# Performance work log

Measured on AMD Instinct MI355X. Metric: run time of the kernel, lower is better.

Reference implementation:

```python
import jax, jax.numpy as jnp
import numpy as np
import math


def _rope(x, cos, sin):
    # x: [B, S, h, hd]; cos/sin: [S, hd//2]
    B, S, h, hd = x.shape
    xr = x.reshape(B, S, h, hd // 2, 2)
    x_re, x_im = xr[..., 0], xr[..., 1]
    c = cos[None, :, None, :]
    s = sin[None, :, None, :]
    out_re = x_re * c - x_im * s
    out_im = x_re * s + x_im * c
    return jnp.stack([out_re, out_im], axis=-1).reshape(B, S, h, hd)


def setup_inputs() -> dict:
    key = jax.random.key(0)
    ks = jax.random.split(key, 8)
    B, S, D = 2, 2048, 2048
    H, G = 16, 4
    hd = D // H  # 128
    q = jax.random.normal(ks[0], (B, S, D), dtype=jnp.float32)
    k = jax.random.normal(ks[1], (B, S, D), dtype=jnp.float32)
    v = jax.random.normal(ks[2], (B, S, D), dtype=jnp.float32)
    # causal mask, matching typical usage (mask==0 -> -inf)
    mask = jnp.broadcast_to(jnp.tril(jnp.ones((S, S), dtype=jnp.int32)), (B, S, S))
    # RoPE freqs: thetas = base**(-2*arange(0,hd,2)/hd), freq = outer(m, thetas)
    exp = -2.0 * jnp.arange(0, hd, 2, dtype=jnp.float32) / hd
    thetas = jnp.power(10000.0, exp)
    m = jnp.arange(S, dtype=jnp.float32)
    freq = jnp.outer(m, thetas)  # [S, hd//2]
    freq_cos = jnp.cos(freq)
    freq_sin = jnp.sin(freq)
    sc = 0.02
    W_q = jax.random.normal(ks[3], (D, D), dtype=jnp.float32) * sc
    W_k = jax.random.normal(ks[4], (D, D // G), dtype=jnp.float32) * sc
    W_v = jax.random.normal(ks[5], (D, D // G), dtype=jnp.float32) * sc
    W_o = jax.random.normal(ks[6], (D, D), dtype=jnp.float32) * sc
    return {"q": q, "k": k, "v": v, "mask": mask, "freq_cos": freq_cos,
            "freq_sin": freq_sin, "W_q": W_q, "W_k": W_k, "W_v": W_v,
            "W_o": W_o, "heads": 16, "group_size": 4}


def reference(q, k, v, mask, freq_cos, freq_sin, W_q, W_k, W_v, W_o, heads, group_size):
    B, S, D = q.shape
    H = heads
    Hkv = H // group_size
    hd = D // H
    qp = (q @ W_q).reshape(B, S, H, hd)
    kp = (k @ W_k).reshape(B, S, Hkv, hd)
    vp = (v @ W_v).reshape(B, S, Hkv, hd)
    qp = _rope(qp, freq_cos, freq_sin)
    kp = _rope(kp, freq_cos, freq_sin)
    # repeat_kv: each kv head repeated group_size times (group index inner)
    kp = jnp.repeat(kp, group_size, axis=2)  # [B,S,H,hd]
    vp = jnp.repeat(vp, group_size, axis=2)
    qh = qp.transpose(0, 2, 1, 3)  # [B,H,S,hd]
    kh = kp.transpose(0, 2, 1, 3)
    vh = vp.transpose(0, 2, 1, 3)
    scores = jnp.einsum('bhqd,bhkd->bhqk', qh, kh) / math.sqrt(hd)
    scores = jnp.where(mask[:, None, :, :] == 0, jnp.float32(-1e9), scores)
    attn = jax.nn.softmax(scores, axis=-1)
    out = jnp.einsum('bhqk,bhkd->bhqd', attn, vh)  # [B,H,S,hd]
    out = out.transpose(0, 2, 1, 3).reshape(B, S, D)
    return out @ W_o
```

## Files before the change

### kernel.cpp

```cpp
#include <hip/hip_runtime.h>

typedef __bf16 bf16;
typedef __attribute__((ext_vector_type(8))) __bf16 bf16x8;
typedef __attribute__((ext_vector_type(4))) __bf16 bf16x4;
typedef __attribute__((ext_vector_type(4))) float f32x4;

#define MFMA16(a, b, c) __builtin_amdgcn_mfma_f32_16x16x32_bf16((a), (b), (c), 0, 0, 0)

typedef __attribute__((address_space(1))) const void* gas_t;
typedef __attribute__((address_space(3))) void* las_t;
#define GLOAD_LDS16(g, l) \
    __builtin_amdgcn_global_load_lds((gas_t)(g), (las_t)(l), 16, 0, 0)

__device__ __forceinline__ unsigned pack2(float a, float b) {
    unsigned short ua = __builtin_bit_cast(unsigned short, (bf16)a);
    unsigned short ub = __builtin_bit_cast(unsigned short, (bf16)b);
    return ((unsigned)ub << 16) | (unsigned)ua;
}

__global__ void transpose_cvt4(const float* __restrict__ Wq,
                               const float* __restrict__ Wo,
                               const float* __restrict__ Wk,
                               const float* __restrict__ Wv,
                               bf16* __restrict__ WqT, bf16* __restrict__ WoT,
                               bf16* __restrict__ WkT, bf16* __restrict__ WvT) {
    __shared__ bf16 tile[32][33];
    int z = blockIdx.z;
    const float* W = (z == 0) ? Wq : (z == 1) ? Wo : (z == 2) ? Wk : Wv;
    bf16* Wt = (z == 0) ? WqT : (z == 1) ? WoT : (z == 2) ? WkT : WvT;
    int N = (z < 2) ? 2048 : 512;
    const int K = 2048;
    int n0 = blockIdx.x * 32;
    if (n0 >= N) return;
    int k0 = blockIdx.y * 32;
    int tx = threadIdx.x, ty = threadIdx.y;
#pragma unroll
    for (int j = 0; j < 4; ++j)
        tile[ty + j * 8][tx] = (bf16)W[(size_t)(k0 + ty + j * 8) * N + n0 + tx];
    __syncthreads();
#pragma unroll
    for (int j = 0; j < 4; ++j)
        Wt[(size_t)(n0 + ty + j * 8) * K + k0 + tx] = tile[tx][ty + j * 8];
}

template <bool A_F32, bool DO_ROPE, int OUT_MODE>
__global__ __launch_bounds__(256) void gemm_bt(
    const void* __restrict__ Ain, const bf16* __restrict__ Bt,
    void* __restrict__ Cout, const float* __restrict__ cosb,
    const float* __restrict__ sinb, float scale, int Nn, int Kk) {
    __shared__ bf16 As[128 * 64];
    __shared__ bf16 Bs[128 * 64];
    int tid = threadIdx.x;
    int lane = tid & 63, wid = tid >> 6;
    int lr = lane & 15, lg = lane >> 4;
    int m0 = blockIdx.y * 128, n0 = blockIdx.x * 128;
    int wr = wid >> 1, wc = wid & 1;

    int srow = lane >> 3;
    int scol = ((lane & 7) ^ srow) << 3;
    const bf16* Bbase = Bt + (size_t)(n0 + wid * 32 + srow) * Kk + scol;
    const bf16* Abase_h =
        A_F32 ? nullptr
              : (const bf16*)Ain + (size_t)(m0 + wid * 32 + srow) * Kk + scol;

    int fragAr = wr * 64 + lr;
    int fragBr = wc * 64 + lr;
    int swz = lr & 7;

    f32x4 acc[4][4] = {};

    const int nk = Kk >> 6;
    for (int kt = 0; kt < nk; ++kt) {
        int k0 = kt << 6;
        if constexpr (A_F32) {
            const float* A = (const float*)Ain;
#pragma unroll
            for (int i = 0; i < 8; ++i) {
                int slot = tid + i * 256;
                int row = slot >> 4, c4 = (slot & 15) << 2;
                f32x4 v = *reinterpret_cast<const f32x4*>(
                    A + (size_t)(m0 + row) * Kk + k0 + c4);
                bf16x4 h;
                h[0] = (bf16)v[0]; h[1] = (bf16)v[1];
                h[2] = (bf16)v[2]; h[3] = (bf16)v[3];
                int blk = (c4 >> 3) ^ (row & 7);
                *reinterpret_cast<bf16x4*>(
                    &As[row * 64 + (blk << 3) + (c4 & 7)]) = h;
            }
        } else {
#pragma unroll
            for (int i = 0; i < 4; ++i)
                GLOAD_LDS16(Abase_h + (size_t)(i * 8) * Kk + k0,
                            &As[(wid * 4 + i) * 512]);
        }
#pragma unroll
        for (int i = 0; i < 4; ++i)
            GLOAD_LDS16(Bbase + (size_t)(i * 8) * Kk + k0,
                        &Bs[(wid * 4 + i) * 512]);
        __syncthreads();
#pragma unroll
        for (int kk = 0; kk < 2; ++kk) {
            int colOff = ((((kk << 2) | lg) ^ swz) << 3);
            bf16x8 af[4], bfr[4];
#pragma unroll
            for (int mi = 0; mi < 4; ++mi)
                af[mi] = *reinterpret_cast<const bf16x8*>(
                    &As[(fragAr + mi * 16) * 64 + colOff]);
#pragma unroll
            for (int ni = 0; ni < 4; ++ni)
                bfr[ni] = *reinterpret_cast<const bf16x8*>(
                    &Bs[(fragBr + ni * 16) * 64 + colOff]);
#pragma unroll
            for (int mi = 0; mi < 4; ++mi)
#pragma unroll
                for (int ni = 0; ni < 4; ++ni)
                    acc[mi][ni] = MFMA16(af[mi], bfr[ni], acc[mi][ni]);
        }
        __syncthreads();
    }

    int m_base = m0 + wr * 64, n_base = n0 + wc * 64;
#pragma unroll
    for (int mi = 0; mi < 4; ++mi) {
#pragma unroll
        for (int ni = 0; ni < 4; ++ni) {
            f32x4 v = acc[mi][ni];
            int gn = n_base + ni * 16 + lr;
            if constexpr (DO_ROPE) {
                int d = gn & 127, p = d >> 1;
                bool ev = ((d & 1) == 0);
#pragma unroll
                for (int r = 0; r < 4; ++r) {
                    int gm = m_base + mi * 16 + lg * 4 + r;
                    int s = gm & 2047;
                    float cc = cosb[s * 64 + p];
                    float ss = sinb[s * 64 + p];
                    float oth = __shfl_xor(v[r], 1);
                    v[r] = (ev ? (v[r] * cc - oth * ss)
                               : (oth * ss + v[r] * cc)) * scale;
                }
            }
            if constexpr (OUT_MODE == 0) {
                bf16* C = (bf16*)Cout;
#pragma unroll
                for (int r = 0; r < 4; ++r)
                    C[(size_t)(m_base + mi * 16 + lg * 4 + r) * Nn + gn] =
                        (bf16)v[r];
            } else {
                float* C = (float*)Cout;
#pragma unroll
                for (int r = 0; r < 4; ++r)
                    C[(size_t)(m_base + mi * 16 + lg * 4 + r) * Nn + gn] = v[r];
            }
        }
    }
}

__global__ __launch_bounds__(256) void gemm_kv(
    const float* __restrict__ kin, const float* __restrict__ vin,
    const bf16* __restrict__ WkT, const bf16* __restrict__ WvT,
    bf16* __restrict__ Kt, bf16* __restrict__ Vt,
    const float* __restrict__ cosb, const float* __restrict__ sinb) {
    const int Nn = 512, Kk = 2048;
    __shared__ bf16 As[128 * 64];
    __shared__ bf16 Bs[128 * 64];
    bool isK = (blockIdx.z == 0);
    const float* A = isK ? kin : vin;
    const bf16* Bt = isK ? WkT : WvT;

    int tid = threadIdx.x;
    int lane = tid & 63, wid = tid >> 6;
    int lr = lane & 15, lg = lane >> 4;
    int m0 = blockIdx.y * 128, n0 = blockIdx.x * 128;
    int wr = wid >> 1, wc = wid & 1;

    int srow = lane >> 3;
    int scol = ((lane & 7) ^ srow) << 3;
    const bf16* Bbase = Bt + (size_t)(n0 + wid * 32 + srow) * Kk + scol;

    int fragAr = wr * 64 + lr;
    int fragBr = wc * 64 + lr;
    int swz = lr & 7;

    f32x4 acc[4][4] = {};

    for (int kt = 0; kt < 32; ++kt) {
        int k0 = kt << 6;
#pragma unroll
        for (int i = 0; i < 8; ++i) {
            int slot = tid + i * 256;
            int row = slot >> 4, c4 = (slot & 15) << 2;
            f32x4 v = *reinterpret_cast<const f32x4*>(
                A + (size_t)(m0 + row) * Kk + k0 + c4);
            bf16x4 h;
            h[0] = (bf16)v[0]; h[1] = (bf16)v[1];
            h[2] = (bf16)v[2]; h[3] = (bf16)v[3];
            int blk = (c4 >> 3) ^ (row & 7);
            *reinterpret_cast<bf16x4*>(&As[row * 64 + (blk << 3) + (c4 & 7)]) = h;
        }
#pragma unroll
        for (int i = 0; i < 4; ++i)
            GLOAD_LDS16(Bbase + (size_t)(i * 8) * Kk + k0,
                        &Bs[(wid * 4 + i) * 512]);
        __syncthreads();
#pragma unroll
        for (int kk = 0; kk < 2; ++kk) {
            int colOff = ((((kk << 2) | lg) ^ swz) << 3);
            bf16x8 af[4], bfr[4];
#pragma unroll
            for (int mi = 0; mi < 4; ++mi)
                af[mi] = *reinterpret_cast<const bf16x8*>(
                    &As[(fragAr + mi * 16) * 64 + colOff]);
#pragma unroll
            for (int ni = 0; ni < 4; ++ni)
                bfr[ni] = *reinterpret_cast<const bf16x8*>(
                    &Bs[(fragBr + ni * 16) * 64 + colOff]);
#pragma unroll
            for (int mi = 0; mi < 4; ++mi)
#pragma unroll
                for (int ni = 0; ni < 4; ++ni)
                    acc[mi][ni] = MFMA16(af[mi], bfr[ni], acc[mi][ni]);
        }
        __syncthreads();
    }

    int m_base = m0 + wr * 64, n_base = n0 + wc * 64;
#pragma unroll
    for (int mi = 0; mi < 4; ++mi) {
#pragma unroll
        for (int ni = 0; ni < 4; ++ni) {
            f32x4 v = acc[mi][ni];
            int gn = n_base + ni * 16 + lr;
            int hkv = gn >> 7, d = gn & 127;
            if (isK) {
                int p = d >> 1;
                bool ev = ((d & 1) == 0);
#pragma unroll
                for (int r = 0; r < 4; ++r) {
                    int gm = m_base + mi * 16 + lg * 4 + r;
                    int s = gm & 2047;
                    float cc = cosb[s * 64 + p];
                    float ss = sinb[s * 64 + p];
                    float oth = __shfl_xor(v[r], 1);
                    float rv = ev ? (v[r] * cc - oth * ss) : (oth * ss + v[r] * cc);
                    int bb = gm >> 11;
                    Kt[((size_t)(bb * 4 + hkv) * 2048 + s) * 128 + d] = (bf16)rv;
                }
            } else {
                int gm0 = m_base + mi * 16 + lg * 4;
                int bb = gm0 >> 11, s = gm0 & 2047;
                bf16x4 hh;
#pragma unroll
                for (int r = 0; r < 4; ++r) hh[r] = (bf16)v[r];
                *reinterpret_cast<bf16x4*>(
                    Vt + ((size_t)(bb * 4 + hkv) * 128 + d) * 2048 + s) = hh;
            }
        }
    }
}

__global__ __launch_bounds__(256) void attn_kernel(
    const bf16* __restrict__ Qp, const bf16* __restrict__ Kt,
    const bf16* __restrict__ Vt, bf16* __restrict__ Ao) {
    const int S = 2048, H = 16, HKV = 4, HD = 128;
    __shared__ bf16 Klds[64][136];
    __shared__ bf16 Vlds[128][72];

    int tid = threadIdx.x, lane = tid & 63, wid = tid >> 6;
    int lr = lane & 15, lg = lane >> 4;
    int h = blockIdx.x, b = blockIdx.y;
    int qt = (int)(gridDim.z - 1) - (int)blockIdx.z;
    int hkv = h >> 2;
    int q0 = qt * 64 + wid * 16;
    int qrow = q0 + lr;

    const bf16* Kbase = Kt + (size_t)(b * HKV + hkv) * S * HD;
    const bf16* Vbase = Vt + (size_t)(b * HKV + hkv) * HD * S;

    bf16x8 qf[4];
    {
        const bf16* qb = Qp + ((size_t)(b * S + qrow) * H + h) * HD;
#pragma unroll
        for (int ks = 0; ks < 4; ++ks)
            qf[ks] = *reinterpret_cast<const bf16x8*>(qb + ks * 32 + lg * 8);
    }

    f32x4 O[8] = {};
    float m_run = -3e38f, l_run = 0.f;
    int src0 = ((lane >> 4) & 1) * 32 + lr;
    int src1 = src0 + 16;
    bool h1 = (lg >> 1) != 0;

    for (int kb = 0; kb <= qt; ++kb) {
        int s0 = kb * 64;
        bf16x8 kreg[4], vreg[4];
#pragma unroll
        for (int i = 0; i < 4; ++i) {
            int slot = tid + i * 256;
            int krow = slot >> 4, kc = (slot & 15) << 3;
            kreg[i] = *reinterpret_cast<const bf16x8*>(
                Kbase + (size_t)(s0 + krow) * HD + kc);
            int vrow = slot >> 3, vc = (slot & 7) << 3;
            vreg[i] = *reinterpret_cast<const bf16x8*>(
                Vbase + (size_t)vrow * S + s0 + vc);
        }
#pragma unroll
        for (int i = 0; i < 4; ++i) {
            int slot = tid + i * 256;
            int krow = slot >> 4, kc = (slot & 15) << 3;
            *reinterpret_cast<bf16x8*>(&Klds[krow][kc]) = kreg[i];
            int vrow = slot >> 3, vc = (slot & 7) << 3;
            *reinterpret_cast<bf16x8*>(&Vlds[vrow][vc]) = vreg[i];
        }
        __syncthreads();

        float p[4][4];
#pragma unroll
        for (int nt = 0; nt < 4; ++nt) {
            f32x4 sc = {};
#pragma unroll
            for (int ks = 0; ks < 4; ++ks) {
                bf16x8 kf = *reinterpret_cast<const bf16x8*>(
                    &Klds[nt * 16 + lr][ks * 32 + lg * 8]);
                sc = MFMA16(kf, qf[ks], sc);
            }
            if (kb == qt) {
                int sa = s0 + nt * 16 + lg * 4;
#pragma unroll
                for (int r = 0; r < 4; ++r)
                    p[nt][r] = (sa + r <= qrow) ? sc[r] : -1e30f;
            } else {
#pragma unroll
                for (int r = 0; r < 4; ++r) p[nt][r] = sc[r];
            }
        }
        float mx = p[0][0];
#pragma unroll
        for (int nt = 0; nt < 4; ++nt)
#pragma unroll
            for (int r = 0; r < 4; ++r) mx = fmaxf(mx, p[nt][r]);
        mx = fmaxf(mx, __shfl_xor(mx, 16));
        mx = fmaxf(mx, __shfl_xor(mx, 32));
        float mnew = fmaxf(m_run, mx);
        float al = __expf(m_run - mnew);
        m_run = mnew;
        float rs = 0.f;
#pragma unroll
        for (int nt = 0; nt < 4; ++nt)
#pragma unroll
            for (int r = 0; r < 4; ++r) {
                p[nt][r] = __expf(p[nt][r] - mnew);
                rs += p[nt][r];
            }
        rs += __shfl_xor(rs, 16);
        rs += __shfl_xor(rs, 32);
        l_run = l_run * al + rs;

        unsigned pk00 = pack2(p[0][0], p[0][1]), pk01 = pack2(p[0][2], p[0][3]);
        unsigned pk10 = pack2(p[1][0], p[1][1]), pk11 = pack2(p[1][2], p[1][3]);
        unsigned pk20 = pack2(p[2][0], p[2][1]), pk21 = pack2(p[2][2], p[2][3]);
        unsigned pk30 = pack2(p[3][0], p[3][1]), pk31 = pack2(p[3][2], p[3][3]);
        unsigned e00 = __shfl(pk00, src0), e01 = __shfl(pk01, src0);
        unsigned e10 = __shfl(pk10, src0), e11 = __shfl(pk11, src0);
        unsigned e20 = __shfl(pk20, src0), e21 = __shfl(pk21, src0);
        unsigned e30 = __shfl(pk30, src0), e31 = __shfl(pk31, src0);
        unsigned o00 = __shfl(pk00, src1), o01 = __shfl(pk01, src1);
        unsigned o10 = __shfl(pk10, src1), o11 = __shfl(pk11, src1);
        unsigned o20 = __shfl(pk20, src1), o21 = __shfl(pk21, src1);
        unsigned o30 = __shfl(pk30, src1), o31 = __shfl(pk31, src1);
        union U { unsigned u[4]; bf16x8 v; } P0, P1;
        P0.u[0] = h1 ? e10 : e00;
        P0.u[1] = h1 ? e11 : e01;
        P0.u[2] = h1 ? o10 : o00;
        P0.u[3] = h1 ? o11 : o01;
        P1.u[0] = h1 ? e30 : e20;
        P1.u[1] = h1 ? e31 : e21;
        P1.u[2] = h1 ? o30 : o20;
        P1.u[3] = h1 ? o31 : o21;

#pragma unroll
        for (int d2 = 0; d2 < 8; ++d2)
#pragma unroll
            for (int r = 0; r < 4; ++r) O[d2][r] *= al;
#pragma unroll
        for (int d2 = 0; d2 < 8; ++d2) {
            bf16x8 vf0 =
                *reinterpret_cast<const bf16x8*>(&Vlds[d2 * 16 + lr][lg * 8]);
            bf16x8 vf1 = *reinterpret_cast<const bf16x8*>(
                &Vlds[d2 * 16 + lr][32 + lg * 8]);
            O[d2] = MFMA16(vf0, P0.v, O[d2]);
            O[d2] = MFMA16(vf1, P1.v, O[d2]);
        }
        __syncthreads();
    }

    float inv = 1.0f / l_run;
    const size_t obase = ((size_t)(b * S + qrow) * H + h) * HD;
#pragma unroll
    for (int d2 = 0; d2 < 8; ++d2) {
        bf16x4 st;
#pragma unroll
        for (int r = 0; r < 4; ++r) st[r] = (bf16)(O[d2][r] * inv);
        *reinterpret_cast<bf16x4*>(const_cast<bf16*>(Ao) + obase + d2 * 16 +
                                   lg * 4) = st;
    }
}

extern "C" void kernel_launch(void* const* d_in, const int* in_sizes, int n_in,
                              void* d_out, int out_size, void* d_ws,
                              size_t ws_size, hipStream_t stream) {
    const float* q = (const float*)d_in[0];
    const float* k = (const float*)d_in[1];
    const float* v = (const float*)d_in[2];
    const float* fc = (const float*)d_in[4];
    const float* fs = (const float*)d_in[5];
    const float* Wq = (const float*)d_in[6];
    const float* Wk = (const float*)d_in[7];
    const float* Wv = (const float*)d_in[8];
    const float* Wo = (const float*)d_in[9];

    char* ws = (char*)d_ws;
    bf16* Wq_t = (bf16*)(ws + 0);
    bf16* Wk_t = (bf16*)(ws + 8388608);
    bf16* Wv_t = (bf16*)(ws + 10485760);
    bf16* Wo_t = (bf16*)(ws + 12582912);
    bf16* Qp   = (bf16*)(ws + 20971520);
    bf16* Kt   = (bf16*)(ws + 37748736);
    bf16* Vt   = (bf16*)(ws + 41943040);
    bf16* Ao   = (bf16*)(ws + 46137344);

    transpose_cvt4<<<dim3(64, 64, 4), dim3(32, 8), 0, stream>>>(
        Wq, Wo, Wk, Wv, Wq_t, Wo_t, Wk_t, Wv_t);

    const float qscale = 0.08838834764831845f;

    gemm_bt<true, true, 0><<<dim3(16, 32), 256, 0, stream>>>(
        (const void*)q, Wq_t, (void*)Qp, fc, fs, qscale, 2048, 2048);
    gemm_kv<<<dim3(4, 32, 2), 256, 0, stream>>>(k, v, Wk_t, Wv_t, Kt, Vt, fc,
                                                fs);

    attn_kernel<<<dim3(16, 2, 32), 256, 0, stream>>>(Qp, Kt, Vt, Ao);

    gemm_bt<false, false, 1><<<dim3(16, 32), 256, 0, stream>>>(
        (const void*)Ao, Wo_t, d_out, fc, fs, 1.0f, 2048, 2048);
}
```

Before: 277.0 us.

## Merge QKV GEMMs into one launch and widen attention tiles with prefetch

The Q, K and V projection GEMMs now run in a single 768-block launch, with mode chosen from the block index, and the output GEMM gets its own bf16-only kernel. The attention kernel now handles 128 query rows per block, 32 per wave as two 16-row sets, so each K/V tile loaded into LDS is reused across more queries. It also prefetches the next K/V tile into registers while the current one is computed, and skips masked or fully visible tiles per wave. Softmax uses exp2 with log2(e) folded into the Q scale. The changes aim to cut launch count, K/V reload traffic and exp cost, at the price of higher register pressure and fewer attention blocks.

```diff
diff --git a/kernel.cpp b/kernel.cpp
--- a/kernel.cpp
+++ b/kernel.cpp
@@ -43,135 +43,38 @@
         Wt[(size_t)(n0 + ty + j * 8) * K + k0 + tx] = tile[tx][ty + j * 8];
 }
 
-template <bool A_F32, bool DO_ROPE, int OUT_MODE>
-__global__ __launch_bounds__(256) void gemm_bt(
-    const void* __restrict__ Ain, const bf16* __restrict__ Bt,
-    void* __restrict__ Cout, const float* __restrict__ cosb,
-    const float* __restrict__ sinb, float scale, int Nn, int Kk) {
+__global__ __launch_bounds__(256) void gemm_qkv(
+    const float* __restrict__ qin, const float* __restrict__ kin,
+    const float* __restrict__ vin, const bf16* __restrict__ WqT,
+    const bf16* __restrict__ WkT, const bf16* __restrict__ WvT,
+    bf16* __restrict__ Qp, bf16* __restrict__ Kt, bf16* __restrict__ Vt,
+    const float* __restrict__ cosb, const float* __restrict__ sinb,
+    float qscale) {
+    const int Kk = 2048;
     __shared__ bf16 As[128 * 64];
     __shared__ bf16 Bs[128 * 64];
+
+    int bid = blockIdx.x;
+    int mode;
+    const float* A;
+    const bf16* Bt;
+    int m0, n0;
+    if (bid < 512) {
+        mode = 0; A = qin; Bt = WqT;
+        n0 = (bid & 15) * 128; m0 = (bid >> 4) * 128;
+    } else if (bid < 640) {
+        int i = bid - 512;
+        mode = 1; A = kin; Bt = WkT;
+        n0 = (i & 3) * 128; m0 = (i >> 2) * 128;
+    } else {
+        int i = bid - 640;
+        mode = 2; A = vin; Bt = WvT;
+        n0 = (i & 3) * 128; m0 = (i >> 2) * 128;
+    }
+
     int tid = threadIdx.x;
     int lane = tid & 63, wid = tid >> 6;
     int lr = lane & 15, lg = lane >> 4;
-    int m0 = blockIdx.y * 128, n0 = blockIdx.x * 128;
-    int wr = wid >> 1, wc = wid & 1;
-
-    int srow = lane >> 3;
-    int scol = ((lane & 7) ^ srow) << 3;
-    const bf16* Bbase = Bt + (size_t)(n0 + wid * 32 + srow) * Kk + scol;
-    const bf16* Abase_h =
-        A_F32 ? nullptr
-              : (const bf16*)Ain + (size_t)(m0 + wid * 32 + srow) * Kk + scol;
-
-    int fragAr = wr * 64 + lr;
-    int fragBr = wc * 64 + lr;
-    int swz = lr & 7;
-
-    f32x4 acc[4][4] = {};
-
-    const int nk = Kk >> 6;
-    for (int kt = 0; kt < nk; ++kt) {
-        int k0 = kt << 6;
-        if constexpr (A_F32) {
-            const float* A = (const float*)Ain;
-#pragma unroll
-            for (int i = 0; i < 8; ++i) {
-                int slot = tid + i * 256;
-                int row = slot >> 4, c4 = (slot & 15) << 2;
-                f32x4 v = *reinterpret_cast<const f32x4*>(
-                    A + (size_t)(m0 + row) * Kk + k0 + c4);
-                bf16x4 h;
-                h[0] = (bf16)v[0]; h[1] = (bf16)v[1];
-                h[2] = (bf16)v[2]; h[3] = (bf16)v[3];
-                int blk = (c4 >> 3) ^ (row & 7);
-                *reinterpret_cast<bf16x4*>(
-                    &As[row * 64 + (blk << 3) + (c4 & 7)]) = h;
-            }
-        } else {
-#pragma unroll
-            for (int i = 0; i < 4; ++i)
-                GLOAD_LDS16(Abase_h + (size_t)(i * 8) * Kk + k0,
-                            &As[(wid * 4 + i) * 512]);
-        }
-#pragma unroll
-        for (int i = 0; i < 4; ++i)
-            GLOAD_LDS16(Bbase + (size_t)(i * 8) * Kk + k0,
-                        &Bs[(wid * 4 + i) * 512]);
-        __syncthreads();
-#pragma unroll
-        for (int kk = 0; kk < 2; ++kk) {
-            int colOff = ((((kk << 2) | lg) ^ swz) << 3);
-            bf16x8 af[4], bfr[4];
-#pragma unroll
-            for (int mi = 0; mi < 4; ++mi)
-                af[mi] = *reinterpret_cast<const bf16x8*>(
-                    &As[(fragAr + mi * 16) * 64 + colOff]);
-#pragma unroll
-            for (int ni = 0; ni < 4; ++ni)
-                bfr[ni] = *reinterpret_cast<const bf16x8*>(
-                    &Bs[(fragBr + ni * 16) * 64 + colOff]);
-#pragma unroll
-            for (int mi = 0; mi < 4; ++mi)
-#pragma unroll
-                for (int ni = 0; ni < 4; ++ni)
-                    acc[mi][ni] = MFMA16(af[mi], bfr[ni], acc[mi][ni]);
-        }
-        __syncthreads();
-    }
-
-    int m_base = m0 + wr * 64, n_base = n0 + wc * 64;
-#pragma unroll
-    for (int mi = 0; mi < 4; ++mi) {
-#pragma unroll
-        for (int ni = 0; ni < 4; ++ni) {
-            f32x4 v = acc[mi][ni];
-            int gn = n_base + ni * 16 + lr;
-            if constexpr (DO_ROPE) {
-                int d = gn & 127, p = d >> 1;
-                bool ev = ((d & 1) == 0);
-#pragma unroll
-                for (int r = 0; r < 4; ++r) {
-                    int gm = m_base + mi * 16 + lg * 4 + r;
-                    int s = gm & 2047;
-                    float cc = cosb[s * 64 + p];
-                    float ss = sinb[s * 64 + p];
-                    float oth = __shfl_xor(v[r], 1);
-                    v[r] = (ev ? (v[r] * cc - oth * ss)
-                               : (oth * ss + v[r] * cc)) * scale;
-                }
-            }
-            if constexpr (OUT_MODE == 0) {
-                bf16* C = (bf16*)Cout;
-#pragma unroll
-                for (int r = 0; r < 4; ++r)
-                    C[(size_t)(m_base + mi * 16 + lg * 4 + r) * Nn + gn] =
-                        (bf16)v[r];
-            } else {
-                float* C = (float*)Cout;
-#pragma unroll
-                for (int r = 0; r < 4; ++r)
-                    C[(size_t)(m_base + mi * 16 + lg * 4 + r) * Nn + gn] = v[r];
-            }
-        }
-    }
-}
-
-__global__ __launch_bounds__(256) void gemm_kv(
-    const float* __restrict__ kin, const float* __restrict__ vin,
-    const bf16* __restrict__ WkT, const bf16* __restrict__ WvT,
-    bf16* __restrict__ Kt, bf16* __restrict__ Vt,
-    const float* __restrict__ cosb, const float* __restrict__ sinb) {
-    const int Nn = 512, Kk = 2048;
-    __shared__ bf16 As[128 * 64];
-    __shared__ bf16 Bs[128 * 64];
-    bool isK = (blockIdx.z == 0);
-    const float* A = isK ? kin : vin;
-    const bf16* Bt = isK ? WkT : WvT;
-
-    int tid = threadIdx.x;
-    int lane = tid & 63, wid = tid >> 6;
-    int lr = lane & 15, lg = lane >> 4;
-    int m0 = blockIdx.y * 128, n0 = blockIdx.x * 128;
     int wr = wid >> 1, wc = wid & 1;
 
     int srow = lane >> 3;
@@ -231,10 +134,11 @@
         for (int ni = 0; ni < 4; ++ni) {
             f32x4 v = acc[mi][ni];
             int gn = n_base + ni * 16 + lr;
-            int hkv = gn >> 7, d = gn & 127;
-            if (isK) {
+            int d = gn & 127;
+            if (mode != 2) {
                 int p = d >> 1;
                 bool ev = ((d & 1) == 0);
+                float sc = (mode == 0) ? qscale : 1.0f;
 #pragma unroll
                 for (int r = 0; r < 4; ++r) {
                     int gm = m_base + mi * 16 + lg * 4 + r;
@@ -242,11 +146,25 @@
                     float cc = cosb[s * 64 + p];
                     float ss = sinb[s * 64 + p];
                     float oth = __shfl_xor(v[r], 1);
-                    float rv = ev ? (v[r] * cc - oth * ss) : (oth * ss + v[r] * cc);
-                    int bb = gm >> 11;
-                    Kt[((size_t)(bb * 4 + hkv) * 2048 + s) * 128 + d] = (bf16)rv;
+                    v[r] = (ev ? (v[r] * cc - oth * ss)
+                               : (oth * ss + v[r] * cc)) * sc;
+                }
+            }
+            if (mode == 0) {
+#pragma unroll
+                for (int r = 0; r < 4; ++r)
+                    Qp[(size_t)(m_base + mi * 16 + lg * 4 + r) * 2048 + gn] =
+                        (bf16)v[r];
+            } else if (mode == 1) {
+                int hkv = gn >> 7;
+#pragma unroll
+                for (int r = 0; r < 4; ++r) {
+                    int gm = m_base + mi * 16 + lg * 4 + r;
+                    int bb = gm >> 11, s = gm & 2047;
+                    Kt[((size_t)(bb * 4 + hkv) * 2048 + s) * 128 + d] = (bf16)v[r];
                 }
             } else {
+                int hkv = gn >> 7;
                 int gm0 = m_base + mi * 16 + lg * 4;
                 int bb = gm0 >> 11, s = gm0 & 2047;
                 bf16x4 hh;
@@ -257,6 +175,73 @@
             }
         }
     }
+}
+
+__global__ __launch_bounds__(256) void gemm_o(
+    const bf16* __restrict__ Ain, const bf16* __restrict__ Bt,
+    float* __restrict__ Cout, int Nn, int Kk) {
+    __shared__ bf16 As[128 * 64];
+    __shared__ bf16 Bs[128 * 64];
+    int tid = threadIdx.x;
+    int lane = tid & 63, wid = tid >> 6;
+    int lr = lane & 15, lg = lane >> 4;
+    int m0 = blockIdx.y * 128, n0 = blockIdx.x * 128;
+    int wr = wid >> 1, wc = wid & 1;
+
+    int srow = lane >> 3;
+    int scol = ((lane & 7) ^ srow) << 3;
+    const bf16* Bbase = Bt + (size_t)(n0 + wid * 32 + srow) * Kk + scol;
+    const bf16* Abase = Ain + (size_t)(m0 + wid * 32 + srow) * Kk + scol;
+
+    int fragAr = wr * 64 + lr;
+    int fragBr = wc * 64 + lr;
+    int swz = lr & 7;
+
+    f32x4 acc[4][4] = {};
+
+    const int nk = Kk >> 6;
+    for (int kt = 0; kt < nk; ++kt) {
+        int k0 = kt << 6;
+#pragma unroll
+        for (int i = 0; i < 4; ++i) {
+            GLOAD_LDS16(Abase + (size_t)(i * 8) * Kk + k0,
+                        &As[(wid * 4 + i) * 512]);
+            GLOAD_LDS16(Bbase + (size_t)(i * 8) * Kk + k0,
+                        &Bs[(wid * 4 + i) * 512]);
+        }
+        __syncthreads();
+#pragma unroll
+        for (int kk = 0; kk < 2; ++kk) {
+            int colOff = ((((kk << 2) | lg) ^ swz) << 3);
+            bf16x8 af[4], bfr[4];
+#pragma unroll
+            for (int mi = 0; mi < 4; ++mi)
+                af[mi] = *reinterpret_cast<const bf16x8*>(
+                    &As[(fragAr + mi * 16) * 64 + colOff]);
+#pragma unroll
+            for (int ni = 0; ni < 4; ++ni)
+                bfr[ni] = *reinterpret_cast<const bf16x8*>(
+                    &Bs[(fragBr + ni * 16) * 64 + colOff]);
+#pragma unroll
+            for (int mi = 0; mi < 4; ++mi)
+#pragma unroll
+                for (int ni = 0; ni < 4; ++ni)
+                    acc[mi][ni] = MFMA16(af[mi], bfr[ni], acc[mi][ni]);
+        }
+        __syncthreads();
+    }
+
+    int m_base = m0 + wr * 64, n_base = n0 + wc * 64;
+#pragma unroll
+    for (int mi = 0; mi < 4; ++mi)
+#pragma unroll
+        for (int ni = 0; ni < 4; ++ni) {
+            f32x4 v = acc[mi][ni];
+            int gn = n_base + ni * 16 + lr;
+#pragma unroll
+            for (int r = 0; r < 4; ++r)
+                Cout[(size_t)(m_base + mi * 16 + lg * 4 + r) * Nn + gn] = v[r];
+        }
 }
 
 __global__ __launch_bounds__(256) void attn_kernel(
@@ -271,138 +256,205 @@
     int h = blockIdx.x, b = blockIdx.y;
     int qt = (int)(gridDim.z - 1) - (int)blockIdx.z;
     int hkv = h >> 2;
-    int q0 = qt * 64 + wid * 16;
-    int qrow = q0 + lr;
+    int q0 = qt * 128 + wid * 32;
+    int qA = q0 + lr, qB = q0 + 16 + lr;
 
     const bf16* Kbase = Kt + (size_t)(b * HKV + hkv) * S * HD;
     const bf16* Vbase = Vt + (size_t)(b * HKV + hkv) * HD * S;
 
-    bf16x8 qf[4];
+    bf16x8 qfA[4], qfB[4];
     {
-        const bf16* qb = Qp + ((size_t)(b * S + qrow) * H + h) * HD;
-#pragma unroll
-        for (int ks = 0; ks < 4; ++ks)
-            qf[ks] = *reinterpret_cast<const bf16x8*>(qb + ks * 32 + lg * 8);
-    }
-
-    f32x4 O[8] = {};
-    float m_run = -3e38f, l_run = 0.f;
+        const bf16* qa = Qp + ((size_t)(b * S + qA) * H + h) * HD;
+        const bf16* qb = Qp + ((size_t)(b * S + qB) * H + h) * HD;
+#pragma unroll
+        for (int ks = 0; ks < 4; ++ks) {
+            qfA[ks] = *reinterpret_cast<const bf16x8*>(qa + ks * 32 + lg * 8);
+            qfB[ks] = *reinterpret_cast<const bf16x8*>(qb + ks * 32 + lg * 8);
+        }
+    }
+
+    f32x4 OA[8] = {}, OB[8] = {};
+    float mA = -3e38f, lA = 0.f, mB = -3e38f, lB = 0.f;
     int src0 = ((lane >> 4) & 1) * 32 + lr;
     int src1 = src0 + 16;
-    bool h1 = (lg >> 1) != 0;
-
-    for (int kb = 0; kb <= qt; ++kb) {
+    bool hi1 = (lg >> 1) != 0;
+
+    int nkb = 2 * qt + 2;
+    bf16x8 kreg[4], vreg[4];
+    int k_r[4], k_c[4], v_r[4], v_c[4];
+#pragma unroll
+    for (int i = 0; i < 4; ++i) {
+        int slot = tid + i * 256;
+        k_r[i] = slot >> 4; k_c[i] = (slot & 15) << 3;
+        v_r[i] = slot >> 3; v_c[i] = (slot & 7) << 3;
+    }
+#pragma unroll
+    for (int i = 0; i < 4; ++i) {
+        kreg[i] = *reinterpret_cast<const bf16x8*>(
+            Kbase + (size_t)k_r[i] * HD + k_c[i]);
+        vreg[i] = *reinterpret_cast<const bf16x8*>(
+            Vbase + (size_t)v_r[i] * S + v_c[i]);
+    }
+
+    for (int kb = 0; kb < nkb; ++kb) {
         int s0 = kb * 64;
-        bf16x8 kreg[4], vreg[4];
 #pragma unroll
         for (int i = 0; i < 4; ++i) {
-            int slot = tid + i * 256;
-            int krow = slot >> 4, kc = (slot & 15) << 3;
-            kreg[i] = *reinterpret_cast<const bf16x8*>(
-                Kbase + (size_t)(s0 + krow) * HD + kc);
-            int vrow = slot >> 3, vc = (slot & 7) << 3;
-            vreg[i] = *reinterpret_cast<const bf16x8*>(
-                Vbase + (size_t)vrow * S + s0 + vc);
-        }
-#pragma unroll
-        for (int i = 0; i < 4; ++i) {
-            int slot = tid + i * 256;
-            int krow = slot >> 4, kc = (slot & 15) << 3;
-            *reinterpret_cast<bf16x8*>(&Klds[krow][kc]) = kreg[i];
-            int vrow = slot >> 3, vc = (slot & 7) << 3;
-            *reinterpret_cast<bf16x8*>(&Vlds[vrow][vc]) = vreg[i];
-        }
-        __syncthreads();
-
-        float p[4][4];
-#pragma unroll
-        for (int nt = 0; nt < 4; ++nt) {
-            f32x4 sc = {};
-#pragma unroll
-            for (int ks = 0; ks < 4; ++ks) {
-                bf16x8 kf = *reinterpret_cast<const bf16x8*>(
-                    &Klds[nt * 16 + lr][ks * 32 + lg * 8]);
-                sc = MFMA16(kf, qf[ks], sc);
-            }
-            if (kb == qt) {
-                int sa = s0 + nt * 16 + lg * 4;
-#pragma unroll
-                for (int r = 0; r < 4; ++r)
-                    p[nt][r] = (sa + r <= qrow) ? sc[r] : -1e30f;
-            } else {
-#pragma unroll
-                for (int r = 0; r < 4; ++r) p[nt][r] = sc[r];
-            }
-        }
-        float mx = p[0][0];
-#pragma unroll
-        for (int nt = 0; nt < 4; ++nt)
-#pragma unroll
-            for (int r = 0; r < 4; ++r) mx = fmaxf(mx, p[nt][r]);
-        mx = fmaxf(mx, __shfl_xor(mx, 16));
-        mx = fmaxf(mx, __shfl_xor(mx, 32));
-        float mnew = fmaxf(m_run, mx);
-        float al = __expf(m_run - mnew);
-        m_run = mnew;
-        float rs = 0.f;
-#pragma unroll
-        for (int nt = 0; nt < 4; ++nt)
-#pragma unroll
-            for (int r = 0; r < 4; ++r) {
-                p[nt][r] = __expf(p[nt][r] - mnew);
-                rs += p[nt][r];
-            }
-        rs += __shfl_xor(rs, 16);
-        rs += __shfl_xor(rs, 32);
-        l_run = l_run * al + rs;
-
-        unsigned pk00 = pack2(p[0][0], p[0][1]), pk01 = pack2(p[0][2], p[0][3]);
-        unsigned pk10 = pack2(p[1][0], p[1][1]), pk11 = pack2(p[1][2], p[1][3]);
-        unsigned pk20 = pack2(p[2][0], p[2][1]), pk21 = pack2(p[2][2], p[2][3]);
-        unsigned pk30 = pack2(p[3][0], p[3][1]), pk31 = pack2(p[3][2], p[3][3]);
-        unsigned e00 = __shfl(pk00, src0), e01 = __shfl(pk01, src0);
-        unsigned e10 = __shfl(pk10, src0), e11 = __shfl(pk11, src0);
-        unsigned e20 = __shfl(pk20, src0), e21 = __shfl(pk21, src0);
-        unsigned e30 = __shfl(pk30, src0), e31 = __shfl(pk31, src0);
-        unsigned o00 = __shfl(pk00, src1), o01 = __shfl(pk01, src1);
-        unsigned o10 = __shfl(pk10, src1), o11 = __shfl(pk11, src1);
-        unsigned o20 = __shfl(pk20, src1), o21 = __shfl(pk21, src1);
-        unsigned o30 = __shfl(pk30, src1), o31 = __shfl(pk31, src1);
-        union U { unsigned u[4]; bf16x8 v; } P0, P1;
-        P0.u[0] = h1 ? e10 : e00;
-        P0.u[1] = h1 ? e11 : e01;
-        P0.u[2] = h1 ? o10 : o00;
-        P0.u[3] = h1 ? o11 : o01;
-        P1.u[0] = h1 ? e30 : e20;
-        P1.u[1] = h1 ? e31 : e21;
-        P1.u[2] = h1 ? o30 : o20;
-        P1.u[3] = h1 ? o31 : o21;
-
-#pragma unroll
-        for (int d2 = 0; d2 < 8; ++d2)
-#pragma unroll
-            for (int r = 0; r < 4; ++r) O[d2][r] *= al;
-#pragma unroll
-        for (int d2 = 0; d2 < 8; ++d2) {
-            bf16x8 vf0 =
-                *reinterpret_cast<const bf16x8*>(&Vlds[d2 * 16 + lr][lg * 8]);
-            bf16x8 vf1 = *reinterpret_cast<const bf16x8*>(
-                &Vlds[d2 * 16 + lr][32 + lg * 8]);
-            O[d2] = MFMA16(vf0, P0.v, O[d2]);
-            O[d2] = MFMA16(vf1, P1.v, O[d2]);
-        }
-        __syncthreads();
-    }
-
-    float inv = 1.0f / l_run;
-    const size_t obase = ((size_t)(b * S + qrow) * H + h) * HD;
+            *reinterpret_cast<bf16x8*>(&Klds[k_r[i]][k_c[i]]) = kreg[i];
+            *reinterpret_cast<bf16x8*>(&Vlds[v_r[i]][v_c[i]]) = vreg[i];
+        }
+        __syncthreads();
+        if (kb + 1 < nkb) {
+            int sn = s0 + 64;
+#pragma unroll
+            for (int i = 0; i < 4; ++i) {
+                kreg[i] = *reinterpret_cast<const bf16x8*>(
+                    Kbase + (size_t)(sn + k_r[i]) * HD + k_c[i]);
+                vreg[i] = *reinterpret_cast<const bf16x8*>(
+                    Vbase + (size_t)v_r[i] * S + sn + v_c[i]);
+            }
+        }
+
+        bool act = (s0 <= q0 + 15);
+        bool full = (q0 - s0 >= 64);
+
+        if (act) {
+            float pA[4][4], pB[4][4];
+#pragma unroll
+            for (int nt = 0; nt < 4; ++nt) {
+                bf16x8 kf[4];
+#pragma unroll
+                for (int ks = 0; ks < 4; ++ks)
+                    kf[ks] = *reinterpret_cast<const bf16x8*>(
+                        &Klds[nt * 16 + lr][ks * 32 + lg * 8]);
+                f32x4 scA = {}, scB = {};
+#pragma unroll
+                for (int ks = 0; ks < 4; ++ks) {
+                    scA = MFMA16(kf[ks], qfA[ks], scA);
+                    scB = MFMA16(kf[ks], qfB[ks], scB);
+                }
+                if (full) {
+#pragma unroll
+                    for (int r = 0; r < 4; ++r) {
+                        pA[nt][r] = scA[r];
+                        pB[nt][r] = scB[r];
+                    }
+                } else {
+                    int sa = s0 + nt * 16 + lg * 4;
+#pragma unroll
+                    for (int r = 0; r < 4; ++r) {
+                        pA[nt][r] = (sa + r <= qA) ? scA[r] : -1e30f;
+                        pB[nt][r] = (sa + r <= qB) ? scB[r] : -1e30f;
+                    }
+                }
+            }
+            float mxA = pA[0][0], mxB = pB[0][0];
+#pragma unroll
+            for (int nt = 0; nt < 4; ++nt)
+#pragma unroll
+                for (int r = 0; r < 4; ++r) {
+                    mxA = fmaxf(mxA, pA[nt][r]);
+                    mxB = fmaxf(mxB, pB[nt][r]);
+                }
+            mxA = fmaxf(mxA, __shfl_xor(mxA, 16));
+            mxA = fmaxf(mxA, __shfl_xor(mxA, 32));
+            mxB = fmaxf(mxB, __shfl_xor(mxB, 16));
+            mxB = fmaxf(mxB, __shfl_xor(mxB, 32));
+            float mnA = fmaxf(mA, mxA), mnB = fmaxf(mB, mxB);
+            float alA = exp2f(mA - mnA), alB = exp2f(mB - mnB);
+            mA = mnA; mB = mnB;
+            float rsA = 0.f, rsB = 0.f;
+#pragma unroll
+            for (int nt = 0; nt < 4; ++nt)
+#pragma unroll
+                for (int r = 0; r < 4; ++r) {
+                    pA[nt][r] = exp2f(pA[nt][r] - mnA);
+                    rsA += pA[nt][r];
+                    pB[nt][r] = exp2f(pB[nt][r] - mnB);
+                    rsB += pB[nt][r];
+                }
+            rsA += __shfl_xor(rsA, 16);
+            rsA += __shfl_xor(rsA, 32);
+            rsB += __shfl_xor(rsB, 16);
+            rsB += __shfl_xor(rsB, 32);
+            lA = lA * alA + rsA;
+            lB = lB * alB + rsB;
+
+            union U { unsigned u[4]; bf16x8 v; } PA0, PA1, PB0, PB1;
+            {
+                unsigned pk00 = pack2(pA[0][0], pA[0][1]), pk01 = pack2(pA[0][2], pA[0][3]);
+                unsigned pk10 = pack2(pA[1][0], pA[1][1]), pk11 = pack2(pA[1][2], pA[1][3]);
+                unsigned pk20 = pack2(pA[2][0], pA[2][1]), pk21 = pack2(pA[2][2], pA[2][3]);
+                unsigned pk30 = pack2(pA[3][0], pA[3][1]), pk31 = pack2(pA[3][2], pA[3][3]);
+                unsigned e00 = __shfl(pk00, src0), e01 = __shfl(pk01, src0);
+                unsigned e10 = __shfl(pk10, src0), e11 = __shfl(pk11, src0);
+                unsigned e20 = __shfl(pk20, src0), e21 = __shfl(pk21, src0);
+                unsigned e30 = __shfl(pk30, src0), e31 = __shfl(pk31, src0);
+                unsigned o00 = __shfl(pk00, src1), o01 = __shfl(pk01, src1);
+                unsigned o10 = __shfl(pk10, src1), o11 = __shfl(pk11, src1);
+                unsigned o20 = __shfl(pk20, src1), o21 = __shfl(pk21, src1);
+                unsigned o30 = __shfl(pk30, src1), o31 = __shfl(pk31, src1);
+                PA0.u[0] = hi1 ? e10 : e00; PA0.u[1] = hi1 ? e11 : e01;
+                PA0.u[2] = hi1 ? o10 : o00; PA0.u[3] = hi1 ? o11 : o01;
+                PA1.u[0] = hi1 ? e30 : e20; PA1.u[1] = hi1 ? e31 : e21;
+                PA1.u[2] = hi1 ? o30 : o20; PA1.u[3] = hi1 ? o31 : o21;
+            }
+            {
+                unsigned pk00 = pack2(pB[0][0], pB[0][1]), pk01 = pack2(pB[0][2], pB[0][3]);
+                unsigned pk10 = pack2(pB[1][0], pB[1][1]), pk11 = pack2(pB[1][2], pB[1][3]);
+                unsigned pk20 = pack2(pB[2][0], pB[2][1]), pk21 = pack2(pB[2][2], pB[2][3]);
+                unsigned pk30 = pack2(pB[3][0], pB[3][1]), pk31 = pack2(pB[3][2], pB[3][3]);
+                unsigned e00 = __shfl(pk00, src0), e01 = __shfl(pk01, src0);
+                unsigned e10 = __shfl(pk10, src0), e11 = __shfl(pk11, src0);
+                unsigned e20 = __shfl(pk20, src0), e21 = __shfl(pk21, src0);
+                unsigned e30 = __shfl(pk30, src0), e31 = __shfl(pk31, src0);
+                unsigned o00 = __shfl(pk00, src1), o01 = __shfl(pk01, src1);
+                unsigned o10 = __shfl(pk10, src1), o11 = __shfl(pk11, src1);
+                unsigned o20 = __shfl(pk20, src1), o21 = __shfl(pk21, src1);
+                unsigned o30 = __shfl(pk30, src1), o31 = __shfl(pk31, src1);
+                PB0.u[0] = hi1 ? e10 : e00; PB0.u[1] = hi1 ? e11 : e01;
+                PB0.u[2] = hi1 ? o10 : o00; PB0.u[3] = hi1 ? o11 : o01;
+                PB1.u[0] = hi1 ? e30 : e20; PB1.u[1] = hi1 ? e31 : e21;
+                PB1.u[2] = hi1 ? o30 : o20; PB1.u[3] = hi1 ? o31 : o21;
+            }
+
+#pragma unroll
+            for (int d2 = 0; d2 < 8; ++d2)
+#pragma unroll
+                for (int r = 0; r < 4; ++r) {
+                    OA[d2][r] *= alA;
+                    OB[d2][r] *= alB;
+                }
+#pragma unroll
+            for (int d2 = 0; d2 < 8; ++d2) {
+                bf16x8 vf0 = *reinterpret_cast<const bf16x8*>(
+                    &Vlds[d2 * 16 + lr][lg * 8]);
+                bf16x8 vf1 = *reinterpret_cast<const bf16x8*>(
+                    &Vlds[d2 * 16 + lr][32 + lg * 8]);
+                OA[d2] = MFMA16(vf0, PA0.v, OA[d2]);
+                OA[d2] = MFMA16(vf1, PA1.v, OA[d2]);
+                OB[d2] = MFMA16(vf0, PB0.v, OB[d2]);
+                OB[d2] = MFMA16(vf1, PB1.v, OB[d2]);
+            }
+        }
+        __syncthreads();
+    }
+
+    float invA = 1.0f / lA, invB = 1.0f / lB;
+    const size_t baseA = ((size_t)(b * S + qA) * H + h) * HD;
+    const size_t baseB = ((size_t)(b * S + qB) * H + h) * HD;
 #pragma unroll
     for (int d2 = 0; d2 < 8; ++d2) {
-        bf16x4 st;
-#pragma unroll
-        for (int r = 0; r < 4; ++r) st[r] = (bf16)(O[d2][r] * inv);
-        *reinterpret_cast<bf16x4*>(const_cast<bf16*>(Ao) + obase + d2 * 16 +
-                                   lg * 4) = st;
+        bf16x4 stA, stB;
+#pragma unroll
+        for (int r = 0; r < 4; ++r) {
+            stA[r] = (bf16)(OA[d2][r] * invA);
+            stB[r] = (bf16)(OB[d2][r] * invB);
+        }
+        *reinterpret_cast<bf16x4*>(const_cast<bf16*>(Ao) + baseA + d2 * 16 +
+                                   lg * 4) = stA;
+        *reinterpret_cast<bf16x4*>(const_cast<bf16*>(Ao) + baseB + d2 * 16 +
+                                   lg * 4) = stB;
     }
 }
 
@@ -432,15 +484,13 @@
     transpose_cvt4<<<dim3(64, 64, 4), dim3(32, 8), 0, stream>>>(
         Wq, Wo, Wk, Wv, Wq_t, Wo_t, Wk_t, Wv_t);
 
-    const float qscale = 0.08838834764831845f;
-
-    gemm_bt<true, true, 0><<<dim3(16, 32), 256, 0, stream>>>(
-        (const void*)q, Wq_t, (void*)Qp, fc, fs, qscale, 2048, 2048);
-    gemm_kv<<<dim3(4, 32, 2), 256, 0, stream>>>(k, v, Wk_t, Wv_t, Kt, Vt, fc,
-                                                fs);
-
-    attn_kernel<<<dim3(16, 2, 32), 256, 0, stream>>>(Qp, Kt, Vt, Ao);
-
-    gemm_bt<false, false, 1><<<dim3(16, 32), 256, 0, stream>>>(
-        (const void*)Ao, Wo_t, d_out, fc, fs, 1.0f, 2048, 2048);
-}
+    const float qscale = 0.08838834764831845f * 1.4426950408889634f;
+
+    gemm_qkv<<<dim3(768), 256, 0, stream>>>(q, k, v, Wq_t, Wk_t, Wv_t, Qp, Kt,
+                                            Vt, fc, fs, qscale);
+
+    attn_kernel<<<dim3(16, 2, 16), 256, 0, stream>>>(Qp, Kt, Vt, Ao);
+
+    gemm_o<<<dim3(16, 32), 256, 0, stream>>>(Ao, Wo_t, (float*)d_out, 2048,
+                                             2048);
+}
```

New measurement: 303.7 us. +9.7%, slower.
